# Kernel optimization log

Hardware: AMD Instinct MI355X
Metric: run time of the kernel (lower is better)

## Reference

```python
import jax, jax.numpy as jnp
import numpy as np

NUM_HEADS = 4
LN_EPS = 1e-5


def setup_inputs() -> dict:
    key = jax.random.key(0)
    B, S, D = 4, 2048, 1024
    H = NUM_HEADS
    hd = D // H
    ks = jax.random.split(key, 8)
    s = 1.0 / np.sqrt(hd)
    inp = {
        "embeddings": jax.random.normal(ks[0], (B, S, D), dtype=jnp.float32),
        # per-head Q/K/V projection weights (torch Linear weight layout [out,in])
        "Wq": jax.random.normal(ks[1], (H, hd, hd), dtype=jnp.float32) * s,
        "Wk": jax.random.normal(ks[2], (H, hd, hd), dtype=jnp.float32) * s,
        "Wv": jax.random.normal(ks[3], (H, hd, hd), dtype=jnp.float32) * s,
        # lens bias scalars: causal, intent, temporal, normative (init values from module)
        "bias_scalars": jnp.array([0.1, 0.15, 0.05, 0.2], dtype=jnp.float32),
        "Wo_w": jax.random.normal(ks[4], (D, D), dtype=jnp.float32) / np.sqrt(D),
        "Wo_b": jnp.zeros((D,), dtype=jnp.float32),
        "ln_g": jnp.ones((D,), dtype=jnp.float32),
        "ln_b": jnp.zeros((D,), dtype=jnp.float32),
    }
    return inp


def _legal_biases(x, bias_scalars):
    """x: [B,H,S,hd] per-head embeddings. Returns stacked bias [B,H,S,S]."""
    B, H, S, hd = x.shape
    # head 0: CAUSAL -> strictly upper triangular mask * causal_bias
    causal = jnp.triu(jnp.ones((S, S), dtype=x.dtype), k=1)  # [S,S]
    b0 = causal[None] * bias_scalars[0]                      # [1,S,S] -> bcast B
    b0 = jnp.broadcast_to(b0, (B, S, S))
    # head 1: INTENTIONALITY -> outer product of embedding norms, global-mean threshold
    mag1 = jnp.linalg.norm(x[:, 1], axis=-1)                 # [B,S]
    intent = mag1[:, :, None] * mag1[:, None, :]             # [B,S,S]
    b1 = (intent > intent.mean()).astype(x.dtype) * bias_scalars[1]
    # head 2: TEMPORAL -> exp(-|i-j|/S)
    pos = jnp.arange(S, dtype=x.dtype)
    prox = jnp.exp(-jnp.abs(pos[:, None] - pos[None, :]) / S)  # [S,S]
    b2 = jnp.broadcast_to(prox[None] * bias_scalars[2], (B, S, S))
    # head 3: NORMATIVE -> outer product of last feature, > 0.5 threshold
    v3 = x[:, 3, :, -1]                                      # [B,S]
    viol = v3[:, :, None] * v3[:, None, :]                   # [B,S,S]
    b3 = (viol > 0.5).astype(x.dtype) * bias_scalars[3]
    return jnp.stack([b0, b1, b2, b3], axis=1)               # [B,H,S,S]


def _forward(embeddings, Wq, Wk, Wv, bias_scalars, Wo_w, Wo_b, ln_g, ln_b):
    B, S, D = embeddings.shape
    H = NUM_HEADS
    hd = D // H
    x = embeddings.reshape(B, S, H, hd).transpose(0, 2, 1, 3)     # [B,H,S,hd]
    # torch Linear: y = x @ W.T
    Q = jnp.einsum('bhsd,hed->bhse', x, Wq)
    K = jnp.einsum('bhsd,hed->bhse', x, Wk)
    V = jnp.einsum('bhsd,hed->bhse', x, Wv)
    scores = jnp.einsum('bhse,bhte->bhst', Q, K) / np.sqrt(hd)    # [B,H,S,S]
    scores = scores + _legal_biases(x, bias_scalars)
    weights = jax.nn.softmax(scores, axis=-1)                     # [B,H,S,S]
    attended = jnp.einsum('bhst,bhte->bhse', weights, V)          # [B,H,S,hd]
    concat = attended.transpose(0, 2, 1, 3).reshape(B, S, D)      # head order = concat order
    out = concat @ Wo_w.T + Wo_b
    # layer_norm(out + embeddings)
    y = out + embeddings
    mu = y.mean(axis=-1, keepdims=True)
    var = ((y - mu) ** 2).mean(axis=-1, keepdims=True)
    output = (y - mu) / jnp.sqrt(var + LN_EPS) * ln_g + ln_b      # [B,S,D]
    average_weights = weights.mean(axis=1)                        # [B,S,S]
    guilt = jax.nn.softmax(average_weights.sum(axis=-1), axis=-1) # [B,S]
    return output, average_weights, guilt


def reference(embeddings, Wq, Wk, Wv, bias_scalars, Wo_w, Wo_b, ln_g, ln_b):
    return _forward(embeddings, Wq, Wk, Wv, bias_scalars, Wo_w, Wo_b, ln_g, ln_b)
```

## Files before the change

### kernel.cpp

```cpp
#include <hip/hip_runtime.h>
#include <hip/hip_bf16.h>
#include <math.h>

#define S_ 2048
#define D_ 1024
#define H_ 4
#define HD_ 256
#define B_ 4

typedef __hip_bfloat16 bf16;
typedef short s16x8 __attribute__((ext_vector_type(8)));
typedef float f32x4 __attribute__((ext_vector_type(4)));

#define GLOAD16(g, l)                                             \
    __builtin_amdgcn_global_load_lds(                             \
        (const __attribute__((address_space(1))) void*)(g),       \
        (__attribute__((address_space(3))) void*)(l), 16, 0, 0)

template <int MODE>
__global__ __launch_bounds__(256) void mfma_nt(
    int K,
    const bf16* __restrict__ A, int lda, long sA_b, long sA_h,
    const bf16* __restrict__ Bm, int ldb, long sB_b, long sB_h,
    void* __restrict__ Cp, int ldc, long sC_b, long sC_h,
    int zdiv, int bbase,
    const double* __restrict__ mag1d, const double* __restrict__ v3d,
    const double* __restrict__ meand, const float* __restrict__ bias_sc)
{
    __shared__ __align__(16) short As[128 * 32];
    __shared__ __align__(16) short Bs[128 * 32];

    const int tid = threadIdx.x;
    const int w = tid >> 6, lane = tid & 63;
    const int srow = lane >> 2, scol = (lane & 3) << 3;
    const int quad = lane >> 4, r = lane & 15;
    const int wr = (w >> 1) * 64, wc = (w & 1) * 64;
    const int zb = blockIdx.z / zdiv, zh = blockIdx.z % zdiv;

    const bf16* Ap = A + (size_t)zb * sA_b + (size_t)zh * sA_h +
                     (size_t)blockIdx.y * 128 * lda;
    const bf16* Bp = Bm + (size_t)zb * sB_b + (size_t)zh * sB_h +
                     (size_t)blockIdx.x * 128 * ldb;

    f32x4 acc[4][4] = {};

    for (int k0 = 0; k0 < K; k0 += 32) {
        if (k0) __syncthreads();
#pragma unroll
        for (int l = 0; l < 2; l++) {
            GLOAD16(Ap + (size_t)(w * 32 + l * 16 + srow) * lda + (k0 + scol),
                    &As[(w * 32 + l * 16) * 32]);
            GLOAD16(Bp + (size_t)(w * 32 + l * 16 + srow) * ldb + (k0 + scol),
                    &Bs[(w * 32 + l * 16) * 32]);
        }
        __syncthreads();

        s16x8 af[4], bfv[4];
        const s16x8* A8 = (const s16x8*)As;
        const s16x8* B8 = (const s16x8*)Bs;
#pragma unroll
        for (int i = 0; i < 4; i++) af[i] = A8[(wr + i * 16 + r) * 4 + quad];
#pragma unroll
        for (int j = 0; j < 4; j++) bfv[j] = B8[(wc + j * 16 + r) * 4 + quad];
#pragma unroll
        for (int i = 0; i < 4; i++)
#pragma unroll
            for (int j = 0; j < 4; j++)
                acc[i][j] = __builtin_amdgcn_mfma_f32_16x16x32_bf16(
                    af[i], bfv[j], acc[i][j], 0, 0, 0);
    }

    const int row0 = blockIdx.y * 128 + wr + quad * 4;
    const int col0 = blockIdx.x * 128 + wc + r;

    if (MODE == 0) {
        float* C = (float*)Cp + (size_t)zb * sC_b + (size_t)zh * sC_h;
#pragma unroll
        for (int i = 0; i < 4; i++)
#pragma unroll
            for (int j = 0; j < 4; j++)
#pragma unroll
                for (int p = 0; p < 4; p++)
                    C[(size_t)(row0 + i * 16 + p) * ldc + (col0 + j * 16)] = acc[i][j][p];
    } else if (MODE == 1) {
        bf16* C = (bf16*)Cp + (size_t)zb * sC_b + (size_t)zh * sC_h;
#pragma unroll
        for (int i = 0; i < 4; i++)
#pragma unroll
            for (int j = 0; j < 4; j++)
#pragma unroll
                for (int p = 0; p < 4; p++)
                    C[(size_t)(row0 + i * 16 + p) * ldc + (col0 + j * 16)] =
                        __float2bfloat16(acc[i][j][p]);
    } else {
        float* C = (float*)Cp + (size_t)zb * sC_b + (size_t)zh * sC_h;
        const int h = zh;
        const int bbatch = bbase + zb;
        const float bsc = bias_sc[h];
        if (h == 0) {
#pragma unroll
            for (int i = 0; i < 4; i++)
#pragma unroll
                for (int j = 0; j < 4; j++)
#pragma unroll
                    for (int p = 0; p < 4; p++) {
                        const int rr = row0 + i * 16 + p, c = col0 + j * 16;
                        C[(size_t)rr * ldc + c] = acc[i][j][p] + ((c > rr) ? bsc : 0.0f);
                    }
        } else if (h == 2) {
#pragma unroll
            for (int i = 0; i < 4; i++)
#pragma unroll
                for (int j = 0; j < 4; j++)
#pragma unroll
                    for (int p = 0; p < 4; p++) {
                        const int rr = row0 + i * 16 + p, c = col0 + j * 16;
                        int d = c - rr; d = d < 0 ? -d : d;
                        C[(size_t)rr * ldc + c] =
                            acc[i][j][p] + bsc * expf(-(float)d * (1.0f / 2048.0f));
                    }
        } else {
            const double* src = (h == 1) ? mag1d : v3d;
            const double thr = (h == 1) ? meand[0] : 0.5;
            double rv[16], cv[4];
#pragma unroll
            for (int i = 0; i < 4; i++)
#pragma unroll
                for (int p = 0; p < 4; p++)
                    rv[i * 4 + p] = src[(size_t)bbatch * S_ + row0 + i * 16 + p];
#pragma unroll
            for (int j = 0; j < 4; j++)
                cv[j] = src[(size_t)bbatch * S_ + col0 + j * 16];
#pragma unroll
            for (int i = 0; i < 4; i++)
#pragma unroll
                for (int j = 0; j < 4; j++)
#pragma unroll
                    for (int p = 0; p < 4; p++) {
                        const int rr = row0 + i * 16 + p, c = col0 + j * 16;
                        C[(size_t)rr * ldc + c] =
                            acc[i][j][p] + ((rv[i * 4 + p] * cv[j] > thr) ? bsc : 0.0f);
                    }
        }
    }
}

__global__ __launch_bounds__(256) void cvt_bf16(const float* __restrict__ in,
                                                bf16* __restrict__ out, int n,
                                                float scale) {
    const size_t i0 = ((size_t)blockIdx.x * 256 + threadIdx.x) * 4;
    if (i0 + 3 < (size_t)n) {
        const float4 v = *(const float4*)(in + i0);
        out[i0 + 0] = __float2bfloat16(v.x * scale);
        out[i0 + 1] = __float2bfloat16(v.y * scale);
        out[i0 + 2] = __float2bfloat16(v.z * scale);
        out[i0 + 3] = __float2bfloat16(v.w * scale);
    }
}

__global__ __launch_bounds__(256) void transpose_v(const bf16* __restrict__ in,
                                                   bf16* __restrict__ out) {
    const int h = blockIdx.z / B_, b = blockIdx.z % B_;
    const int e0 = blockIdx.x * 64, s0 = blockIdx.y * 64;
    __shared__ short t[64][66];
    const int tid = threadIdx.x;
    const int rr = tid >> 2;
    const int cc = (tid & 3) << 4;
    const bf16* ip = in + (((size_t)h * B_ * S_) + (size_t)b * S_ + s0) * HD_ + e0;
    const s16x8 v0 = *(const s16x8*)(ip + (size_t)rr * HD_ + cc);
    const s16x8 v1 = *(const s16x8*)(ip + (size_t)rr * HD_ + cc + 8);
#pragma unroll
    for (int i = 0; i < 8; i++) {
        t[rr][cc + i] = v0[i];
        t[rr][cc + 8 + i] = v1[i];
    }
    __syncthreads();
    bf16* op = out + (((size_t)h * B_ + b) * HD_ + e0 + rr) * S_ + s0 + cc;
    s16x8 o0, o1;
#pragma unroll
    for (int i = 0; i < 8; i++) {
        o0[i] = t[cc + i][rr];
        o1[i] = t[cc + 8 + i][rr];
    }
    *(s16x8*)op = o0;
    *(s16x8*)(op + 8) = o1;
}

__global__ __launch_bounds__(256) void prep_kernel(const float* __restrict__ emb,
                                                   double* __restrict__ mag1d,
                                                   double* __restrict__ v3d) {
    const long row = blockIdx.x;
    const int tid = threadIdx.x;
    const float x = emb[row * D_ + 256 + tid];
    __shared__ double red[256];
    red[tid] = (double)x * (double)x;
    __syncthreads();
    for (int off = 128; off > 0; off >>= 1) {
        if (tid < off) red[tid] += red[tid + off];
        __syncthreads();
    }
    if (tid == 0) {
        mag1d[row] = sqrt(red[0]);
        v3d[row] = (double)emb[row * D_ + 1023];
    }
}

__global__ __launch_bounds__(256) void mean_kernel(const double* __restrict__ mag1d,
                                                   double* __restrict__ meand) {
    const int tid = threadIdx.x;
    __shared__ double red[256];
    double acc = 0.0;
    for (int b = 0; b < B_; b++) {
        double ss = 0.0;
        for (int i = tid; i < S_; i += 256) ss += mag1d[(long)b * S_ + i];
        __syncthreads();
        red[tid] = ss;
        __syncthreads();
        for (int off = 128; off > 0; off >>= 1) {
            if (tid < off) red[tid] += red[tid + off];
            __syncthreads();
        }
        if (tid == 0) {
            const double rb = red[0] / (double)S_;
            acc += rb * rb;
        }
        __syncthreads();
    }
    if (tid == 0) meand[0] = acc / (double)B_;
}

__global__ __launch_bounds__(256) void softmax_fused(
    const float* __restrict__ scores, bf16* __restrict__ P, long p_h, int p_row,
    float* __restrict__ avgw, float* __restrict__ rowsum) {
    const int s = blockIdx.x, tid = threadIdx.x;
    __shared__ float red[256];
    float wacc[8] = {0, 0, 0, 0, 0, 0, 0, 0};
    for (int h = 0; h < H_; h++) {
        const float* rp = scores + ((size_t)h * S_ + s) * S_;
        bf16* pp = P + (size_t)h * p_h + (size_t)s * p_row;
        float v[8];
        float m = -1e30f;
#pragma unroll
        for (int i = 0; i < 8; i++) {
            v[i] = rp[tid + 256 * i];
            m = fmaxf(m, v[i]);
        }
        red[tid] = m;
        __syncthreads();
        for (int off = 128; off > 0; off >>= 1) {
            if (tid < off) red[tid] = fmaxf(red[tid], red[tid + off]);
            __syncthreads();
        }
        m = red[0];
        __syncthreads();
        float sum = 0.0f;
#pragma unroll
        for (int i = 0; i < 8; i++) {
            v[i] = expf(v[i] - m);
            sum += v[i];
        }
        red[tid] = sum;
        __syncthreads();
        for (int off = 128; off > 0; off >>= 1) {
            if (tid < off) red[tid] += red[tid + off];
            __syncthreads();
        }
        const float inv = 1.0f / red[0];
        __syncthreads();
#pragma unroll
        for (int i = 0; i < 8; i++) {
            const float wv = v[i] * inv;
            pp[tid + 256 * i] = __float2bfloat16(wv);
            wacc[i] += wv;
        }
    }
    float asum = 0.0f;
#pragma unroll
    for (int i = 0; i < 8; i++) {
        const float a = wacc[i] * 0.25f;
        avgw[(size_t)s * S_ + tid + 256 * i] = a;
        asum += a;
    }
    red[tid] = asum;
    __syncthreads();
    for (int off = 128; off > 0; off >>= 1) {
        if (tid < off) red[tid] += red[tid + off];
        __syncthreads();
    }
    if (tid == 0) rowsum[s] = red[0];
}

__global__ __launch_bounds__(256) void ln_kernel(float* __restrict__ out,
                                                 const float* __restrict__ emb,
                                                 const float* __restrict__ wob,
                                                 const float* __restrict__ g,
                                                 const float* __restrict__ beta) {
    const long row = blockIdx.x;
    float* o = out + row * D_;
    const float* e = emb + row * D_;
    const int tid = threadIdx.x;
    __shared__ float red[256];
    float v[4];
    float sum = 0.0f;
#pragma unroll
    for (int i = 0; i < 4; i++) {
        const int c = tid + 256 * i;
        v[i] = o[c] + wob[c] + e[c];
        sum += v[i];
    }
    red[tid] = sum;
    __syncthreads();
    for (int off = 128; off > 0; off >>= 1) {
        if (tid < off) red[tid] += red[tid + off];
        __syncthreads();
    }
    const float mu = red[0] * (1.0f / 1024.0f);
    __syncthreads();
    float vs = 0.0f;
#pragma unroll
    for (int i = 0; i < 4; i++) {
        const float d = v[i] - mu;
        vs += d * d;
    }
    red[tid] = vs;
    __syncthreads();
    for (int off = 128; off > 0; off >>= 1) {
        if (tid < off) red[tid] += red[tid + off];
        __syncthreads();
    }
    const float var = red[0] * (1.0f / 1024.0f);
    const float inv = 1.0f / sqrtf(var + 1e-5f);
#pragma unroll
    for (int i = 0; i < 4; i++) {
        const int c = tid + 256 * i;
        o[c] = (v[i] - mu) * inv * g[c] + beta[c];
    }
}

__global__ __launch_bounds__(256) void guilt_kernel(const float* __restrict__ rowsum,
                                                    float* __restrict__ guilt) {
    const int b = blockIdx.x, tid = threadIdx.x;
    const float* r = rowsum + (long)b * S_;
    float* gq = guilt + (long)b * S_;
    __shared__ float red[256];
    float v[8];
    float m = -1e30f;
#pragma unroll
    for (int i = 0; i < 8; i++) {
        v[i] = r[tid + 256 * i];
        m = fmaxf(m, v[i]);
    }
    red[tid] = m;
    __syncthreads();
    for (int off = 128; off > 0; off >>= 1) {
        if (tid < off) red[tid] = fmaxf(red[tid], red[tid + off]);
        __syncthreads();
    }
    m = red[0];
    __syncthreads();
    float sum = 0.0f;
#pragma unroll
    for (int i = 0; i < 8; i++) {
        v[i] = expf(v[i] - m);
        sum += v[i];
    }
    red[tid] = sum;
    __syncthreads();
    for (int off = 128; off > 0; off >>= 1) {
        if (tid < off) red[tid] += red[tid + off];
        __syncthreads();
    }
    const float inv = 1.0f / red[0];
#pragma unroll
    for (int i = 0; i < 8; i++) gq[tid + 256 * i] = v[i] * inv;
}

extern "C" void kernel_launch(void* const* d_in, const int* in_sizes, int n_in,
                              void* d_out, int out_size, void* d_ws, size_t ws_size,
                              hipStream_t stream) {
    const float* emb = (const float*)d_in[0];
    const float* Wq = (const float*)d_in[1];
    const float* Wk = (const float*)d_in[2];
    const float* Wv = (const float*)d_in[3];
    const float* bias_sc = (const float*)d_in[4];
    const float* Wo_w = (const float*)d_in[5];
    const float* Wo_b = (const float*)d_in[6];
    const float* ln_g = (const float*)d_in[7];
    const float* ln_bt = (const float*)d_in[8];

    char* ws = (char*)d_ws;
    size_t off = 0;
    auto alloc = [&](size_t bytes) {
        size_t o = off;
        off = (off + bytes + 255) & ~(size_t)255;
        return o;
    };
    bf16* embb = (bf16*)(ws + alloc((size_t)B_ * S_ * D_ * 2));
    bf16* concat = embb;
    bf16* Qm = (bf16*)(ws + alloc((size_t)H_ * B_ * S_ * HD_ * 2));
    bf16* Km = (bf16*)(ws + alloc((size_t)H_ * B_ * S_ * HD_ * 2));
    bf16* Vtb = (bf16*)(ws + alloc((size_t)H_ * B_ * HD_ * S_ * 2));
    bf16* Wqb = (bf16*)(ws + alloc((size_t)H_ * HD_ * HD_ * 2));
    bf16* Wkb = (bf16*)(ws + alloc((size_t)H_ * HD_ * HD_ * 2));
    bf16* Wvb = (bf16*)(ws + alloc((size_t)H_ * HD_ * HD_ * 2));
    bf16* Wob = (bf16*)(ws + alloc((size_t)D_ * D_ * 2));
    double* mag1d = (double*)(ws + alloc((size_t)B_ * S_ * 8));
    double* v3d = (double*)(ws + alloc((size_t)B_ * S_ * 8));
    double* meand = (double*)(ws + alloc(256));
    float* rowsum = (float*)(ws + alloc((size_t)B_ * S_ * 4));
    float* scores = (float*)(ws + alloc((size_t)H_ * S_ * S_ * 4));
    bf16* Vraw = (bf16*)scores;
    bf16* P = (bf16*)(ws + off);
    const size_t need_batched = off + (size_t)B_ * H_ * S_ * S_ * 2;
    const bool batched = ws_size >= need_batched;

    float* outp = (float*)d_out;
    float* avgw = outp + (size_t)B_ * S_ * D_;
    float* guilt = avgw + (size_t)B_ * S_ * S_;

    cvt_bf16<<<(B_ * S_ * D_) / 1024, 256, 0, stream>>>(emb, embb, B_ * S_ * D_, 1.0f);
    cvt_bf16<<<(H_ * HD_ * HD_) / 1024, 256, 0, stream>>>(Wq, Wqb, H_ * HD_ * HD_, 0.0625f);
    cvt_bf16<<<(H_ * HD_ * HD_) / 1024, 256, 0, stream>>>(Wk, Wkb, H_ * HD_ * HD_, 1.0f);
    cvt_bf16<<<(H_ * HD_ * HD_) / 1024, 256, 0, stream>>>(Wv, Wvb, H_ * HD_ * HD_, 1.0f);
    cvt_bf16<<<(D_ * D_) / 1024, 256, 0, stream>>>(Wo_w, Wob, D_ * D_, 1.0f);

    prep_kernel<<<B_ * S_, 256, 0, stream>>>(emb, mag1d, v3d);
    mean_kernel<<<1, 256, 0, stream>>>(mag1d, meand);

    {
        const dim3 g(HD_ / 128, (B_ * S_) / 128, H_);
        const long sQ = (long)B_ * S_ * HD_;
        mfma_nt<1><<<g, 256, 0, stream>>>(HD_, embb, D_, 0, HD_,
                                          Wqb, HD_, 0, (long)HD_ * HD_,
                                          Qm, HD_, 0, sQ, H_, 0,
                                          nullptr, nullptr, nullptr, nullptr);
        mfma_nt<1><<<g, 256, 0, stream>>>(HD_, embb, D_, 0, HD_,
                                          Wkb, HD_, 0, (long)HD_ * HD_,
                                          Km, HD_, 0, sQ, H_, 0,
                                          nullptr, nullptr, nullptr, nullptr);
        mfma_nt<1><<<g, 256, 0, stream>>>(HD_, embb, D_, 0, HD_,
                                          Wvb, HD_, 0, (long)HD_ * HD_,
                                          Vraw, HD_, 0, sQ, H_, 0,
                                          nullptr, nullptr, nullptr, nullptr);
    }
    transpose_v<<<dim3(HD_ / 64, S_ / 64, H_ * B_), 256, 0, stream>>>(Vraw, Vtb);

    for (int b = 0; b < B_; b++) {
        mfma_nt<3><<<dim3(S_ / 128, S_ / 128, H_), 256, 0, stream>>>(
            HD_,
            Qm + (size_t)b * S_ * HD_, HD_, 0, (long)B_ * S_ * HD_,
            Km + (size_t)b * S_ * HD_, HD_, 0, (long)B_ * S_ * HD_,
            scores, S_, 0, (long)S_ * S_,
            H_, b, mag1d, v3d, meand, bias_sc);
        if (batched) {
            softmax_fused<<<S_, 256, 0, stream>>>(
                scores, P + (size_t)b * H_ * S_ * S_, (long)S_ * S_, S_,
                avgw + (size_t)b * S_ * S_, rowsum + (size_t)b * S_);
        } else {
            softmax_fused<<<S_, 256, 0, stream>>>(
                scores, (bf16*)scores, 2L * S_ * S_, 2 * S_,
                avgw + (size_t)b * S_ * S_, rowsum + (size_t)b * S_);
            mfma_nt<1><<<dim3(HD_ / 128, S_ / 128, H_), 256, 0, stream>>>(
                S_,
                (const bf16*)scores, 2 * S_, 0, 2L * S_ * S_,
                Vtb + (size_t)b * HD_ * S_, S_, 0, (long)B_ * HD_ * S_,
                concat + (size_t)b * S_ * D_, D_, 0, HD_,
                H_, 0, nullptr, nullptr, nullptr, nullptr);
        }
    }
    if (batched) {
        mfma_nt<1><<<dim3(HD_ / 128, S_ / 128, B_ * H_), 256, 0, stream>>>(
            S_,
            P, S_, (long)H_ * S_ * S_, (long)S_ * S_,
            Vtb, S_, (long)HD_ * S_, (long)B_ * HD_ * S_,
            concat, D_, (long)S_ * D_, HD_,
            H_, 0, nullptr, nullptr, nullptr, nullptr);
    }

    mfma_nt<0><<<dim3(D_ / 128, (B_ * S_) / 128, 1), 256, 0, stream>>>(
        D_, concat, D_, 0, 0, Wob, D_, 0, 0, outp, D_, 0, 0,
        1, 0, nullptr, nullptr, nullptr, nullptr);

    ln_kernel<<<B_ * S_, 256, 0, stream>>>(outp, emb, Wo_b, ln_g, ln_bt);
    guilt_kernel<<<B_, 256, 0, stream>>>(rowsum, guilt);
}
```

Measured before the change: 522.9 us.

## Stage score epilogue through LDS, process two softmax rows per block, add wide PV GEMM

The score GEMM epilogue now stages each 16-row accumulator slice through shared memory, so the bias add and the stores go out as row-contiguous float4 writes instead of scattered scalar stores. The softmax kernel handles two rows per block with paired reductions, which halves block count and amortises barrier cost. The batched P·V product moves to a new 512-thread kernel with 128x256 tiles, so each P tile is loaded once across the full head dimension. These add extra barriers in the epilogue and larger shared-memory use per block.

```diff
diff --git a/kernel.cpp b/kernel.cpp
--- a/kernel.cpp
+++ b/kernel.cpp
@@ -27,8 +27,9 @@
     const double* __restrict__ mag1d, const double* __restrict__ v3d,
     const double* __restrict__ meand, const float* __restrict__ bias_sc)
 {
-    __shared__ __align__(16) short As[128 * 32];
-    __shared__ __align__(16) short Bs[128 * 32];
+    __shared__ __align__(16) float smem_f[32 * 132];
+    short* As = (short*)smem_f;
+    short* Bs = As + 128 * 32;
 
     const int tid = threadIdx.x;
     const int w = tid >> 6, lane = tid & 63;
@@ -97,52 +98,100 @@
         const int h = zh;
         const int bbatch = bbase + zb;
         const float bsc = bias_sc[h];
-        if (h == 0) {
-#pragma unroll
-            for (int i = 0; i < 4; i++)
-#pragma unroll
-                for (int j = 0; j < 4; j++)
-#pragma unroll
-                    for (int p = 0; p < 4; p++) {
-                        const int rr = row0 + i * 16 + p, c = col0 + j * 16;
-                        C[(size_t)rr * ldc + c] = acc[i][j][p] + ((c > rr) ? bsc : 0.0f);
+        const double* src = (h == 1) ? mag1d : v3d;
+        const double thr = (h == 1) ? meand[0] : 0.5;
+        const int lrbase = (w >> 1) * 16 + quad * 4;
+        float* ep = smem_f;
+#pragma unroll
+        for (int i = 0; i < 4; i++) {
+            __syncthreads();
+#pragma unroll
+            for (int j = 0; j < 4; j++)
+#pragma unroll
+                for (int p = 0; p < 4; p++)
+                    ep[(lrbase + p) * 132 + wc + j * 16 + r] = acc[i][j][p];
+            __syncthreads();
+#pragma unroll
+            for (int it = 0; it < 4; it++) {
+                const int fidx = it * 256 + tid;
+                const int lr = fidx >> 5, c4 = (fidx & 31) * 4;
+                const int rr = blockIdx.y * 128 + (lr >> 4) * 64 + i * 16 + (lr & 15);
+                const int cc0 = blockIdx.x * 128 + c4;
+                float4 v = *(float4*)&ep[lr * 132 + c4];
+                float bias[4];
+                if (h == 0) {
+#pragma unroll
+                    for (int q = 0; q < 4; q++) bias[q] = (cc0 + q > rr) ? bsc : 0.0f;
+                } else if (h == 2) {
+#pragma unroll
+                    for (int q = 0; q < 4; q++) {
+                        int d = cc0 + q - rr; d = d < 0 ? -d : d;
+                        bias[q] = bsc * expf(-(float)d * (1.0f / 2048.0f));
                     }
-        } else if (h == 2) {
-#pragma unroll
-            for (int i = 0; i < 4; i++)
-#pragma unroll
-                for (int j = 0; j < 4; j++)
-#pragma unroll
-                    for (int p = 0; p < 4; p++) {
-                        const int rr = row0 + i * 16 + p, c = col0 + j * 16;
-                        int d = c - rr; d = d < 0 ? -d : d;
-                        C[(size_t)rr * ldc + c] =
-                            acc[i][j][p] + bsc * expf(-(float)d * (1.0f / 2048.0f));
-                    }
-        } else {
-            const double* src = (h == 1) ? mag1d : v3d;
-            const double thr = (h == 1) ? meand[0] : 0.5;
-            double rv[16], cv[4];
-#pragma unroll
-            for (int i = 0; i < 4; i++)
-#pragma unroll
-                for (int p = 0; p < 4; p++)
-                    rv[i * 4 + p] = src[(size_t)bbatch * S_ + row0 + i * 16 + p];
+                } else {
+                    const double rv = src[(size_t)bbatch * S_ + rr];
+#pragma unroll
+                    for (int q = 0; q < 4; q++)
+                        bias[q] = (rv * src[(size_t)bbatch * S_ + cc0 + q] > thr)
+                                      ? bsc : 0.0f;
+                }
+                v.x += bias[0]; v.y += bias[1]; v.z += bias[2]; v.w += bias[3];
+                *(float4*)&C[(size_t)rr * ldc + cc0] = v;
+            }
+        }
+    }
+}
+
+__global__ __launch_bounds__(512) void pv_gemm(const bf16* __restrict__ P,
+                                               const bf16* __restrict__ Vt,
+                                               bf16* __restrict__ concat) {
+    __shared__ __align__(16) short As[128 * 32];
+    __shared__ __align__(16) short Bs[256 * 32];
+    const int tid = threadIdx.x;
+    const int w = tid >> 6, lane = tid & 63;
+    const int srow = lane >> 2, scol = (lane & 3) << 3;
+    const int quad = lane >> 4, r = lane & 15;
+    const int wy = w >> 2, wx = w & 3;
+    const int z = blockIdx.y, b = z >> 2, h = z & 3;
+    const bf16* Ap = P + (size_t)z * S_ * S_ + (size_t)blockIdx.x * 128 * S_;
+    const bf16* Bp = Vt + ((size_t)h * B_ + b) * HD_ * S_;
+
+    f32x4 acc[4][4] = {};
+
+    for (int k0 = 0; k0 < S_; k0 += 32) {
+        if (k0) __syncthreads();
+        GLOAD16(Ap + (size_t)(w * 16 + srow) * S_ + (k0 + scol), &As[(w * 16) * 32]);
+        GLOAD16(Bp + (size_t)(w * 16 + srow) * S_ + (k0 + scol), &Bs[(w * 16) * 32]);
+        GLOAD16(Bp + (size_t)(128 + w * 16 + srow) * S_ + (k0 + scol),
+                &Bs[(128 + w * 16) * 32]);
+        __syncthreads();
+
+        s16x8 af[4], bfv[4];
+        const s16x8* A8 = (const s16x8*)As;
+        const s16x8* B8 = (const s16x8*)Bs;
+#pragma unroll
+        for (int i = 0; i < 4; i++) af[i] = A8[(wy * 64 + i * 16 + r) * 4 + quad];
+#pragma unroll
+        for (int j = 0; j < 4; j++) bfv[j] = B8[(wx * 64 + j * 16 + r) * 4 + quad];
+#pragma unroll
+        for (int i = 0; i < 4; i++)
 #pragma unroll
             for (int j = 0; j < 4; j++)
-                cv[j] = src[(size_t)bbatch * S_ + col0 + j * 16];
-#pragma unroll
-            for (int i = 0; i < 4; i++)
-#pragma unroll
-                for (int j = 0; j < 4; j++)
-#pragma unroll
-                    for (int p = 0; p < 4; p++) {
-                        const int rr = row0 + i * 16 + p, c = col0 + j * 16;
-                        C[(size_t)rr * ldc + c] =
-                            acc[i][j][p] + ((rv[i * 4 + p] * cv[j] > thr) ? bsc : 0.0f);
-                    }
-        }
-    }
+                acc[i][j] = __builtin_amdgcn_mfma_f32_16x16x32_bf16(
+                    af[i], bfv[j], acc[i][j], 0, 0, 0);
+    }
+
+    const int row0 = blockIdx.x * 128 + wy * 64 + quad * 4;
+    const int col0 = wx * 64 + r;
+    bf16* C = concat + (size_t)b * S_ * D_ + h * HD_;
+#pragma unroll
+    for (int i = 0; i < 4; i++)
+#pragma unroll
+        for (int j = 0; j < 4; j++)
+#pragma unroll
+            for (int p = 0; p < 4; p++)
+                C[(size_t)(row0 + i * 16 + p) * D_ + (col0 + j * 16)] =
+                    __float2bfloat16(acc[i][j][p]);
 }
 
 __global__ __launch_bounds__(256) void cvt_bf16(const float* __restrict__ in,
@@ -229,65 +278,92 @@
     if (tid == 0) meand[0] = acc / (double)B_;
 }
 
-__global__ __launch_bounds__(256) void softmax_fused(
-    const float* __restrict__ scores, bf16* __restrict__ P, long p_h, int p_row,
+__global__ __launch_bounds__(256) void softmax2(
+    const float* __restrict__ scores, bf16* __restrict__ P, long p_h, long p_row,
     float* __restrict__ avgw, float* __restrict__ rowsum) {
-    const int s = blockIdx.x, tid = threadIdx.x;
-    __shared__ float red[256];
-    float wacc[8] = {0, 0, 0, 0, 0, 0, 0, 0};
+    const int s0 = blockIdx.x * 2, tid = threadIdx.x;
+    __shared__ float2 red[256];
+    float wa0[8] = {0, 0, 0, 0, 0, 0, 0, 0};
+    float wa1[8] = {0, 0, 0, 0, 0, 0, 0, 0};
     for (int h = 0; h < H_; h++) {
-        const float* rp = scores + ((size_t)h * S_ + s) * S_;
-        bf16* pp = P + (size_t)h * p_h + (size_t)s * p_row;
-        float v[8];
-        float m = -1e30f;
+        const float* r0 = scores + ((size_t)h * S_ + s0) * S_;
+        const float* r1 = r0 + S_;
+        float v0[8], v1[8];
+        float m0 = -1e30f, m1 = -1e30f;
 #pragma unroll
         for (int i = 0; i < 8; i++) {
-            v[i] = rp[tid + 256 * i];
-            m = fmaxf(m, v[i]);
-        }
-        red[tid] = m;
+            v0[i] = r0[tid + 256 * i];
+            m0 = fmaxf(m0, v0[i]);
+            v1[i] = r1[tid + 256 * i];
+            m1 = fmaxf(m1, v1[i]);
+        }
+        red[tid] = make_float2(m0, m1);
         __syncthreads();
         for (int off = 128; off > 0; off >>= 1) {
-            if (tid < off) red[tid] = fmaxf(red[tid], red[tid + off]);
+            if (tid < off) {
+                red[tid].x = fmaxf(red[tid].x, red[tid + off].x);
+                red[tid].y = fmaxf(red[tid].y, red[tid + off].y);
+            }
             __syncthreads();
         }
-        m = red[0];
-        __syncthreads();
-        float sum = 0.0f;
+        m0 = red[0].x;
+        m1 = red[0].y;
+        __syncthreads();
+        float s0s = 0.0f, s1s = 0.0f;
 #pragma unroll
         for (int i = 0; i < 8; i++) {
-            v[i] = expf(v[i] - m);
-            sum += v[i];
-        }
-        red[tid] = sum;
+            v0[i] = expf(v0[i] - m0);
+            s0s += v0[i];
+            v1[i] = expf(v1[i] - m1);
+            s1s += v1[i];
+        }
+        red[tid] = make_float2(s0s, s1s);
         __syncthreads();
         for (int off = 128; off > 0; off >>= 1) {
-            if (tid < off) red[tid] += red[tid + off];
+            if (tid < off) {
+                red[tid].x += red[tid + off].x;
+                red[tid].y += red[tid + off].y;
+            }
             __syncthreads();
         }
-        const float inv = 1.0f / red[0];
-        __syncthreads();
+        const float inv0 = 1.0f / red[0].x;
+        const float inv1 = 1.0f / red[0].y;
+        __syncthreads();
+        bf16* p0 = P + (size_t)h * p_h + (size_t)s0 * p_row;
+        bf16* p1 = p0 + p_row;
 #pragma unroll
         for (int i = 0; i < 8; i++) {
-            const float wv = v[i] * inv;
-            pp[tid + 256 * i] = __float2bfloat16(wv);
-            wacc[i] += wv;
-        }
-    }
-    float asum = 0.0f;
+            const float w0 = v0[i] * inv0;
+            p0[tid + 256 * i] = __float2bfloat16(w0);
+            wa0[i] += w0;
+            const float w1 = v1[i] * inv1;
+            p1[tid + 256 * i] = __float2bfloat16(w1);
+            wa1[i] += w1;
+        }
+    }
+    float as0 = 0.0f, as1 = 0.0f;
 #pragma unroll
     for (int i = 0; i < 8; i++) {
-        const float a = wacc[i] * 0.25f;
-        avgw[(size_t)s * S_ + tid + 256 * i] = a;
-        asum += a;
-    }
-    red[tid] = asum;
+        const float a0 = wa0[i] * 0.25f;
+        avgw[(size_t)s0 * S_ + tid + 256 * i] = a0;
+        as0 += a0;
+        const float a1 = wa1[i] * 0.25f;
+        avgw[(size_t)(s0 + 1) * S_ + tid + 256 * i] = a1;
+        as1 += a1;
+    }
+    red[tid] = make_float2(as0, as1);
     __syncthreads();
     for (int off = 128; off > 0; off >>= 1) {
-        if (tid < off) red[tid] += red[tid + off];
-        __syncthreads();
-    }
-    if (tid == 0) rowsum[s] = red[0];
+        if (tid < off) {
+            red[tid].x += red[tid + off].x;
+            red[tid].y += red[tid + off].y;
+        }
+        __syncthreads();
+    }
+    if (tid == 0) {
+        rowsum[s0] = red[0].x;
+        rowsum[s0 + 1] = red[0].y;
+    }
 }
 
 __global__ __launch_bounds__(256) void ln_kernel(float* __restrict__ out,
@@ -453,11 +529,11 @@
             scores, S_, 0, (long)S_ * S_,
             H_, b, mag1d, v3d, meand, bias_sc);
         if (batched) {
-            softmax_fused<<<S_, 256, 0, stream>>>(
+            softmax2<<<S_ / 2, 256, 0, stream>>>(
                 scores, P + (size_t)b * H_ * S_ * S_, (long)S_ * S_, S_,
                 avgw + (size_t)b * S_ * S_, rowsum + (size_t)b * S_);
         } else {
-            softmax_fused<<<S_, 256, 0, stream>>>(
+            softmax2<<<S_ / 2, 256, 0, stream>>>(
                 scores, (bf16*)scores, 2L * S_ * S_, 2 * S_,
                 avgw + (size_t)b * S_ * S_, rowsum + (size_t)b * S_);
             mfma_nt<1><<<dim3(HD_ / 128, S_ / 128, H_), 256, 0, stream>>>(
@@ -469,12 +545,7 @@
         }
     }
     if (batched) {
-        mfma_nt<1><<<dim3(HD_ / 128, S_ / 128, B_ * H_), 256, 0, stream>>>(
-            S_,
-            P, S_, (long)H_ * S_ * S_, (long)S_ * S_,
-            Vtb, S_, (long)HD_ * S_, (long)B_ * HD_ * S_,
-            concat, D_, (long)S_ * D_, HD_,
-            H_, 0, nullptr, nullptr, nullptr, nullptr);
+        pv_gemm<<<dim3(S_ / 128, B_ * H_), 512, 0, stream>>>(P, Vtb, concat);
     }
 
     mfma_nt<0><<<dim3(D_ / 128, (B_ * S_) / 128, 1), 256, 0, stream>>>(
```

Result: no change. 531.6 us (+1.7%).
